# Kernel optimization log

Measured on AMD Instinct MI355X. Metric: run time of the kernel, lower is better.

## Reference

```python
import jax, jax.numpy as jnp
import numpy as np

BN_EPS = 1e-5


def setup_inputs() -> dict:
    key = jax.random.key(0)
    ks = jax.random.split(key, 5)
    B, C, T, V = 64, 64, 300, 25
    O, N = 128, 8  # out_channels, num_adj
    x = jax.random.normal(ks[0], (B, C, T, V), dtype=jnp.float32)
    # adjacency: row-normalized so powers A^1..A^8 stay well-conditioned
    A = jax.random.uniform(ks[1], (V, V), dtype=jnp.float32)
    A = A / jnp.sum(A, axis=1, keepdims=True)
    W = jax.random.normal(ks[2], (N, O // N, C), dtype=jnp.float32) * 0.05  # per-branch 1x1 conv weights
    Wr = jax.random.normal(ks[3], (O, C), dtype=jnp.float32) * 0.05          # residual 1x1 conv weight
    br = jnp.zeros((O,), dtype=jnp.float32)                                   # residual conv bias
    gamma = jnp.ones((O,), dtype=jnp.float32)
    beta = jnp.zeros((O,), dtype=jnp.float32)
    return {"x": x, "A": A, "W": W, "Wr": Wr, "br": br, "gamma": gamma, "beta": beta}


def reference(x, A, W, Wr, br, gamma, beta):
    # x: [B, C, T, V]; A: [V, V]; W: [num_adj, O//num_adj, C]
    num_adj = W.shape[0]
    outs = []
    A_pow = A  # A_list[i] = A^(i+1), matching _split_adjacency_matrix
    for i in range(num_adj):
        g = jnp.einsum('bcfj,jk->bcfk', x, A_pow)           # graph conv on joints
        outs.append(jnp.einsum('oc,bcfk->bofk', W[i], g))   # 1x1 conv (no bias)
        A_pow = A_pow @ A
    out = jnp.concatenate(outs, axis=1)                      # [B, O, T, V]
    residual = jnp.einsum('oc,bcfj->bofj', Wr, x) + br[None, :, None, None]
    out = out + residual
    # BatchNorm2d (training-mode batch statistics over B, T, V per channel)
    mean = jnp.mean(out, axis=(0, 2, 3), keepdims=True)
    var = jnp.var(out, axis=(0, 2, 3), keepdims=True)
    out = gamma[None, :, None, None] * (out - mean) / jnp.sqrt(var + BN_EPS) + beta[None, :, None, None]
    return jax.nn.relu(out)
```

## Files before the change

### kernel.cpp

```cpp
#include <hip/hip_runtime.h>
#include <hip/hip_bf16.h>

#define B_  64
#define C_  64
#define T_  300
#define V_  25
#define O_  128
#define TV  (T_*V_)
#define BTV (B_*T_*V_)
#define NPF 4800
#define HS_STRIDE 258
#define HS_ROWS 107

typedef __bf16 bf16x8 __attribute__((ext_vector_type(8)));
typedef float f32x4 __attribute__((ext_vector_type(4)));

#define WSB_AF    0ull
#define WSB_WT    18432ull
#define WSB_PSC   51200ull
#define WSB_PSQ   2508800ull
#define WSB_P2C   4966400ull
#define WSB_P2Q   5015552ull
#define WSB_SCL   5064704ull
#define WSB_SFT   5065216ull
#define WSB_Y     5065728ull
#define WS_NEED2  127945728ull

static __device__ __forceinline__ unsigned short f2bf(float f) {
    unsigned int u = __float_as_uint(f);
    unsigned int r = (u + 0x7fffu + ((u >> 16) & 1u)) >> 16;
    return (unsigned short)r;
}
static __device__ __forceinline__ float bf2f(unsigned short u) {
    return __uint_as_float(((unsigned int)u) << 16);
}

__global__ __launch_bounds__(256) void k_prep(const float* __restrict__ A,
                                              const float* __restrict__ W,
                                              const float* __restrict__ Wr,
                                              unsigned short* __restrict__ AF,
                                              unsigned short* __restrict__ Wt) {
    const int tid = threadIdx.x;
    if (blockIdx.x == 0) {
        __shared__ float Pall[8][625];
        for (int p = tid; p < 625; p += 256) Pall[0][p] = A[p];
        __syncthreads();
        for (int i = 1; i < 8; i++) {
            for (int p = tid; p < 625; p += 256) {
                int r = p / 25, c = p - r * 25;
                float s = 0.f;
                #pragma unroll 5
                for (int j = 0; j < 25; j++) s = fmaf(Pall[i-1][r*25 + j], A[j*25 + c], s);
                Pall[i][p] = s;
            }
            __syncthreads();
        }
        for (int idx = tid; idx < 18 * 64; idx += 256) {
            int fi = idx >> 6, l = idx & 63, qq = l >> 4, tt = l & 15;
            unsigned short v[8];
            #pragma unroll
            for (int e = 0; e < 8; e++) {
                int j = qq * 8 + e;
                float val = 0.f;
                if (fi < 16) {
                    int i = fi >> 1, k = (fi & 1) * 16 + tt;
                    if (j < 25 && k < 25) val = Pall[i][j * 25 + k];
                } else {
                    int k = (fi - 16) * 16 + tt;
                    if (j < 25 && k < 25 && j == k) val = 1.f;
                }
                v[e] = f2bf(val);
            }
            *(uint4*)(AF + idx * 8) = *(uint4*)v;
        }
    } else {
        const int oc = tid;
        const float* src = (oc < 128) ? (W + oc * 64) : (Wr + (oc - 128) * 64);
        unsigned short row[64];
        #pragma unroll
        for (int c = 0; c < 64; c++) row[c] = f2bf(src[c]);
        #pragma unroll
        for (int cc = 0; cc < 8; cc++)
            *(uint4*)(Wt + oc * 64 + cc * 8) = *(uint4*)(row + cc * 8);
    }
}

__global__ __launch_bounds__(512, 2) void k_fuse(const float* __restrict__ x,
                                                 const unsigned short* __restrict__ Wt,
                                                 const unsigned short* __restrict__ AF,
                                                 unsigned short* __restrict__ Yg,
                                                 float* __restrict__ psc,
                                                 float* __restrict__ psq) {
    __shared__ __align__(16) unsigned short SM[8192 + HS_ROWS * HS_STRIDE];
    unsigned short* As = SM;
    unsigned short* Hs = SM + 8192;
    const int tg = blockIdx.x, b = blockIdx.y;
    const int tid = threadIdx.x, wv = tid >> 6, ln = tid & 63;
    const int q = ln >> 4, t = ln & 15;

    for (int p = tid; p < 1600; p += 512) {
        int c = p / 25, e4 = p - c * 25;
        float4 f = *(const float4*)(x + ((size_t)(b * 64 + c)) * TV + tg * 100 + e4 * 4);
        float vv[4] = { f.x, f.y, f.z, f.w };
        #pragma unroll
        for (int u = 0; u < 4; u++) {
            int r = e4 * 4 + u;
            As[r * 64 + (((c >> 3) ^ (r & 7)) << 3) + (c & 7)] = f2bf(vv[u]);
        }
    }
    for (int w = tid; w < 896; w += 512) ((unsigned int*)As)[3200 + w] = 0u;
    for (int w = tid; w < 903; w += 512) ((unsigned int*)Hs)[12900 + w] = 0u;
    __syncthreads();

    {
        const int rb = wv >> 2, oq = wv & 3;
        f32x4 acc[4][4] = {};
        #pragma unroll
        for (int ks = 0; ks < 2; ks++) {
            const unsigned short* wb = Wt + (oq * 64 + t) * 64 + q * 8 + ks * 32;
            bf16x8 bv[4], af[4];
            #pragma unroll
            for (int ni = 0; ni < 4; ni++) bv[ni] = *(const bf16x8*)(wb + ni * 1024);
            #pragma unroll
            for (int mi = 0; mi < 4; mi++) {
                int row = rb * 64 + mi * 16 + t;
                af[mi] = *(const bf16x8*)(As + row * 64 + (((ks * 4 + q) ^ (row & 7)) << 3));
            }
            #pragma unroll
            for (int mi = 0; mi < 4; mi++)
                #pragma unroll
                for (int ni = 0; ni < 4; ni++)
                    acc[mi][ni] = __builtin_amdgcn_mfma_f32_16x16x32_bf16(bv[ni], af[mi], acc[mi][ni], 0, 0, 0);
        }
        #pragma unroll
        for (int mi = 0; mi < 4; mi++) {
            int row = rb * 64 + mi * 16 + t;
            if (row < 100) {
                #pragma unroll
                for (int ni = 0; ni < 4; ni++) {
                    int co = oq * 64 + ni * 16 + q * 4;
                    unsigned int* dst = (unsigned int*)(Hs + row * HS_STRIDE + co);
                    dst[0] = (unsigned int)f2bf(acc[mi][ni][0]) | ((unsigned int)f2bf(acc[mi][ni][1]) << 16);
                    dst[1] = (unsigned int)f2bf(acc[mi][ni][2]) | ((unsigned int)f2bf(acc[mi][ni][3]) << 16);
                }
            }
        }
    }
    __syncthreads();

    const int s = wv >> 1, bh = wv & 1;
    const bf16x8* AFp = (const bf16x8*)AF;
    const bf16x8 id0 = AFp[16 * 64 + ln];
    const bf16x8 id1 = AFp[17 * 64 + ln];
    f32x4 acc2[4][2];
    #pragma unroll
    for (int ii = 0; ii < 4; ii++) { acc2[ii][0] = (f32x4){0,0,0,0}; acc2[ii][1] = (f32x4){0,0,0,0}; }
    const int rowq = (s * 25 + q * 8) * HS_STRIDE + t;
    #pragma unroll
    for (int ii = 0; ii < 4; ii++) {
        const int i = bh * 4 + ii;
        unsigned short hm[8], hr[8];
        #pragma unroll
        for (int e = 0; e < 8; e++) {
            int a = rowq + e * HS_STRIDE + i * 16;
            hm[e] = Hs[a];
            hr[e] = Hs[a + 128];
        }
        bf16x8 bm = *(bf16x8*)hm;
        bf16x8 brs = *(bf16x8*)hr;
        bf16x8 a0 = AFp[(i * 2 + 0) * 64 + ln];
        bf16x8 a1 = AFp[(i * 2 + 1) * 64 + ln];
        acc2[ii][0] = __builtin_amdgcn_mfma_f32_16x16x32_bf16(id0, brs, acc2[ii][0], 0, 0, 0);
        acc2[ii][1] = __builtin_amdgcn_mfma_f32_16x16x32_bf16(id1, brs, acc2[ii][1], 0, 0, 0);
        acc2[ii][0] = __builtin_amdgcn_mfma_f32_16x16x32_bf16(a0, bm, acc2[ii][0], 0, 0, 0);
        acc2[ii][1] = __builtin_amdgcn_mfma_f32_16x16x32_bf16(a1, bm, acc2[ii][1], 0, 0, 0);
    }
    float* ps = (float*)SM;
    float* qs = ps + 512;
    #pragma unroll
    for (int ii = 0; ii < 4; ii++) {
        float si = 0.f, qi = 0.f;
        #pragma unroll
        for (int mt = 0; mt < 2; mt++)
            #pragma unroll
            for (int r = 0; r < 4; r++) {
                float v = acc2[ii][mt][r];
                si += v; qi += v * v;
            }
        si += __shfl_xor(si, 16); si += __shfl_xor(si, 32);
        qi += __shfl_xor(qi, 16); qi += __shfl_xor(qi, 32);
        if (ln < 16) {
            ps[s * 128 + (bh * 4 + ii) * 16 + t] = si;
            qs[s * 128 + (bh * 4 + ii) * 16 + t] = qi;
        }
    }
    #pragma unroll
    for (int ii = 0; ii < 4; ii++)
        #pragma unroll
        for (int mt = 0; mt < 2; mt++)
            #pragma unroll
            for (int r = 0; r < 4; r++) {
                int k = mt * 16 + q * 4 + r;
                if (k < 25)
                    Hs[(s * 25 + k) * HS_STRIDE + (bh * 4 + ii) * 16 + t] = f2bf(acc2[ii][mt][r]);
            }
    __syncthreads();
    if (tid < 128) {
        float S = ps[tid] + ps[128 + tid] + ps[256 + tid] + ps[384 + tid];
        float Q = qs[tid] + qs[128 + tid] + qs[256 + tid] + qs[384 + tid];
        int blk = b * 75 + tg;
        psc[(size_t)blk * 128 + tid] = S;
        psq[(size_t)blk * 128 + tid] = Q;
    }
    for (int idx = tid; idx < 3200; idx += 512) {
        int o = idx / 25, w = idx - o * 25;
        unsigned short vv[4];
        #pragma unroll
        for (int e = 0; e < 4; e++)
            vv[e] = Hs[(w * 4 + e) * HS_STRIDE + o];
        uint2 d;
        d.x = (unsigned int)vv[0] | ((unsigned int)vv[1] << 16);
        d.y = (unsigned int)vv[2] | ((unsigned int)vv[3] << 16);
        *(uint2*)(Yg + (size_t)(b * 128 + o) * TV + tg * 100 + w * 4) = d;
    }
}

__global__ __launch_bounds__(256) void k_red1(const float* __restrict__ psc,
                                              const float* __restrict__ psq,
                                              float* __restrict__ p2c,
                                              float* __restrict__ p2q) {
    const int r = blockIdx.x;
    const int tid = threadIdx.x;
    const int o = tid & 127;
    const float* src = (tid < 128) ? psc : psq;
    float* dst = (tid < 128) ? p2c : p2q;
    float S = 0.f;
    for (int ii = 0; ii < 50; ii++)
        S += src[(size_t)(r * 50 + ii) * 128 + o];
    dst[r * 128 + o] = S;
}

__global__ void k_fin(const float* __restrict__ p2c, const float* __restrict__ p2q,
                      const float* __restrict__ gamma, const float* __restrict__ beta,
                      float* __restrict__ scale, float* __restrict__ shift) {
    const int o = threadIdx.x;
    if (o >= 128) return;
    float S = 0.f, Q = 0.f;
    for (int r = 0; r < 96; r++) { S += p2c[r * 128 + o]; Q += p2q[r * 128 + o]; }
    float inv = 1.f / (float)BTV;
    float mean = S * inv;
    float var = Q * inv - mean * mean;
    float sc = gamma[o] / sqrtf(var + 1e-5f);
    scale[o] = sc;
    shift[o] = beta[o] - mean * sc;
}

__global__ __launch_bounds__(256) void k_norm2(const unsigned short* __restrict__ Y,
                                               const float* __restrict__ scale,
                                               const float* __restrict__ shift,
                                               float* __restrict__ out) {
    size_t e0 = ((size_t)blockIdx.x * 256 + threadIdx.x) * 8;
    #pragma unroll
    for (int g = 0; g < 2; g++) {
        size_t e = e0 + (size_t)g * 4;
        int o = (int)((e / 7500) & 127);
        float sc = scale[o], sh = shift[o];
        uint2 v = *(const uint2*)(Y + e);
        float4 d;
        d.x = fmaxf(fmaf(bf2f((unsigned short)(v.x & 0xffffu)), sc, sh), 0.f);
        d.y = fmaxf(fmaf(bf2f((unsigned short)(v.x >> 16)),     sc, sh), 0.f);
        d.z = fmaxf(fmaf(bf2f((unsigned short)(v.y & 0xffffu)), sc, sh), 0.f);
        d.w = fmaxf(fmaf(bf2f((unsigned short)(v.y >> 16)),     sc, sh), 0.f);
        *(float4*)(out + e) = d;
    }
}

extern "C" void kernel_launch(void* const* d_in, const int* in_sizes, int n_in,
                              void* d_out, int out_size, void* d_ws, size_t ws_size,
                              hipStream_t stream) {
    const float* x     = (const float*)d_in[0];
    const float* A     = (const float*)d_in[1];
    const float* W     = (const float*)d_in[2];
    const float* Wr    = (const float*)d_in[3];
    const float* gamma = (const float*)d_in[5];
    const float* beta  = (const float*)d_in[6];
    float* out = (float*)d_out;
    char* wsb  = (char*)d_ws;
    if (ws_size < (size_t)WS_NEED2) return;

    unsigned short* AF  = (unsigned short*)(wsb + WSB_AF);
    unsigned short* Wt  = (unsigned short*)(wsb + WSB_WT);
    float*          psc = (float*)(wsb + WSB_PSC);
    float*          psq = (float*)(wsb + WSB_PSQ);
    float*          p2c = (float*)(wsb + WSB_P2C);
    float*          p2q = (float*)(wsb + WSB_P2Q);
    float*          scl = (float*)(wsb + WSB_SCL);
    float*          sft = (float*)(wsb + WSB_SFT);
    unsigned short* Y   = (unsigned short*)(wsb + WSB_Y);

    k_prep<<<2, 256, 0, stream>>>(A, W, Wr, AF, Wt);
    k_fuse<<<dim3(75, 64), 512, 0, stream>>>(x, Wt, AF, Y, psc, psq);
    k_red1<<<96, 256, 0, stream>>>(psc, psq, p2c, p2q);
    k_fin<<<1, 128, 0, stream>>>(p2c, p2q, gamma, beta, scl, sft);
    k_norm2<<<30000, 256, 0, stream>>>(Y, scl, sft, out);
}
```

Measured before the change: 220.3 us.

## Fuse conv, BN statistics and normalization into one cooperative persistent kernel

Replaces the four-kernel pipeline (fused conv, two-stage stats reduction, finalize, normalize) with one cooperative kernel of 480 persistent blocks, each handling 10 tiles. Each block keeps its bf16 conv outputs in registers, writes partial BN sums, crosses a grid-wide barrier, reduces the statistics itself, then normalizes and writes the output. This removes the bf16 intermediate Y round-trip through global memory and three kernel launches. In exchange it adds heavy register pressure from holding 10 tiles of results, needs 480 blocks co-resident under launch bounds of 4 blocks per CU, and pays for a grid sync. If the cooperative launch fails, it falls back to the old kernels.

```diff
diff --git a/kernel.cpp b/kernel.cpp
--- a/kernel.cpp
+++ b/kernel.cpp
@@ -1,5 +1,8 @@
 #include <hip/hip_runtime.h>
 #include <hip/hip_bf16.h>
+#include <hip/hip_cooperative_groups.h>
+
+namespace cg = cooperative_groups;
 
 #define B_  64
 #define C_  64
@@ -8,9 +11,10 @@
 #define O_  128
 #define TV  (T_*V_)
 #define BTV (B_*T_*V_)
-#define NPF 4800
 #define HS_STRIDE 258
 #define HS_ROWS 107
+#define NBLK 480
+#define TILES_PB 10
 
 typedef __bf16 bf16x8 __attribute__((ext_vector_type(8)));
 typedef float f32x4 __attribute__((ext_vector_type(4)));
@@ -82,6 +86,201 @@
         #pragma unroll
         for (int cc = 0; cc < 8; cc++)
             *(uint4*)(Wt + oc * 64 + cc * 8) = *(uint4*)(row + cc * 8);
+    }
+}
+
+__global__ __launch_bounds__(512, 4) void k_mega(const float* __restrict__ x,
+                                                 const unsigned short* __restrict__ Wt,
+                                                 const unsigned short* __restrict__ AF,
+                                                 const float* __restrict__ gamma,
+                                                 const float* __restrict__ beta,
+                                                 float* __restrict__ psc,
+                                                 float* __restrict__ psq,
+                                                 float* __restrict__ out) {
+    __shared__ __align__(16) unsigned short SM[8192 + HS_ROWS * HS_STRIDE];
+    __shared__ float scl[128], sft[128];
+    unsigned short* As = SM;
+    unsigned short* Hs = SM + 8192;
+    const int tid = threadIdx.x, wv = tid >> 6, ln = tid & 63;
+    const int q = ln >> 4, t = ln & 15;
+    const int s = wv >> 1, bh = wv & 1;
+    const bf16x8* AFp = (const bf16x8*)AF;
+    const bf16x8 id0 = AFp[16 * 64 + ln];
+    const bf16x8 id1 = AFp[17 * 64 + ln];
+    const int tile0 = blockIdx.x * TILES_PB;
+
+    for (int w = tid; w < 896; w += 512) ((unsigned int*)As)[3200 + w] = 0u;
+    for (int w = tid; w < 903; w += 512) ((unsigned int*)Hs)[12900 + w] = 0u;
+
+    float sacc[4] = {0.f, 0.f, 0.f, 0.f}, qacc[4] = {0.f, 0.f, 0.f, 0.f};
+    uint2 y[TILES_PB][4][2];
+
+    #pragma unroll
+    for (int tl = 0; tl < TILES_PB; tl++) {
+        const int tile = tile0 + tl;
+        const int b = tile / 75, tg = tile - b * 75;
+        __syncthreads();
+        for (int p = tid; p < 1600; p += 512) {
+            int c = p / 25, e4 = p - c * 25;
+            float4 f = *(const float4*)(x + ((size_t)(b * 64 + c)) * TV + tg * 100 + e4 * 4);
+            float vv[4] = { f.x, f.y, f.z, f.w };
+            #pragma unroll
+            for (int u = 0; u < 4; u++) {
+                int r = e4 * 4 + u;
+                As[r * 64 + (((c >> 3) ^ (r & 7)) << 3) + (c & 7)] = f2bf(vv[u]);
+            }
+        }
+        __syncthreads();
+        {
+            const int rb = wv >> 2, oq = wv & 3;
+            f32x4 acc[4][4] = {};
+            #pragma unroll
+            for (int ks = 0; ks < 2; ks++) {
+                const unsigned short* wb = Wt + (oq * 64 + t) * 64 + q * 8 + ks * 32;
+                bf16x8 bv[4], af[4];
+                #pragma unroll
+                for (int ni = 0; ni < 4; ni++) bv[ni] = *(const bf16x8*)(wb + ni * 1024);
+                #pragma unroll
+                for (int mi = 0; mi < 4; mi++) {
+                    int row = rb * 64 + mi * 16 + t;
+                    af[mi] = *(const bf16x8*)(As + row * 64 + (((ks * 4 + q) ^ (row & 7)) << 3));
+                }
+                #pragma unroll
+                for (int mi = 0; mi < 4; mi++)
+                    #pragma unroll
+                    for (int ni = 0; ni < 4; ni++)
+                        acc[mi][ni] = __builtin_amdgcn_mfma_f32_16x16x32_bf16(bv[ni], af[mi], acc[mi][ni], 0, 0, 0);
+            }
+            #pragma unroll
+            for (int mi = 0; mi < 4; mi++) {
+                int row = rb * 64 + mi * 16 + t;
+                if (row < 100) {
+                    #pragma unroll
+                    for (int ni = 0; ni < 4; ni++) {
+                        int co = oq * 64 + ni * 16 + q * 4;
+                        unsigned int* dst = (unsigned int*)(Hs + row * HS_STRIDE + co);
+                        dst[0] = (unsigned int)f2bf(acc[mi][ni][0]) | ((unsigned int)f2bf(acc[mi][ni][1]) << 16);
+                        dst[1] = (unsigned int)f2bf(acc[mi][ni][2]) | ((unsigned int)f2bf(acc[mi][ni][3]) << 16);
+                    }
+                }
+            }
+        }
+        __syncthreads();
+        {
+            f32x4 acc2[4][2];
+            #pragma unroll
+            for (int ii = 0; ii < 4; ii++) { acc2[ii][0] = (f32x4){0,0,0,0}; acc2[ii][1] = (f32x4){0,0,0,0}; }
+            const int rowq = (s * 25 + q * 8) * HS_STRIDE + t;
+            #pragma unroll
+            for (int ii = 0; ii < 4; ii++) {
+                const int i = bh * 4 + ii;
+                unsigned short hm[8], hr[8];
+                #pragma unroll
+                for (int e = 0; e < 8; e++) {
+                    int a = rowq + e * HS_STRIDE + i * 16;
+                    hm[e] = Hs[a];
+                    hr[e] = Hs[a + 128];
+                }
+                bf16x8 bm = *(bf16x8*)hm;
+                bf16x8 brs = *(bf16x8*)hr;
+                bf16x8 a0 = AFp[(i * 2 + 0) * 64 + ln];
+                bf16x8 a1 = AFp[(i * 2 + 1) * 64 + ln];
+                acc2[ii][0] = __builtin_amdgcn_mfma_f32_16x16x32_bf16(id0, brs, acc2[ii][0], 0, 0, 0);
+                acc2[ii][1] = __builtin_amdgcn_mfma_f32_16x16x32_bf16(id1, brs, acc2[ii][1], 0, 0, 0);
+                acc2[ii][0] = __builtin_amdgcn_mfma_f32_16x16x32_bf16(a0, bm, acc2[ii][0], 0, 0, 0);
+                acc2[ii][1] = __builtin_amdgcn_mfma_f32_16x16x32_bf16(a1, bm, acc2[ii][1], 0, 0, 0);
+            }
+            #pragma unroll
+            for (int ii = 0; ii < 4; ii++) {
+                float si = 0.f, qi = 0.f;
+                #pragma unroll
+                for (int mt = 0; mt < 2; mt++) {
+                    #pragma unroll
+                    for (int r = 0; r < 4; r++) {
+                        float v = acc2[ii][mt][r];
+                        si += v; qi += v * v;
+                    }
+                    y[tl][ii][mt].x = (unsigned int)f2bf(acc2[ii][mt][0]) | ((unsigned int)f2bf(acc2[ii][mt][1]) << 16);
+                    y[tl][ii][mt].y = (unsigned int)f2bf(acc2[ii][mt][2]) | ((unsigned int)f2bf(acc2[ii][mt][3]) << 16);
+                }
+                sacc[ii] += si; qacc[ii] += qi;
+            }
+        }
+    }
+
+    __syncthreads();
+    float* ps = (float*)SM;
+    float* qs = ps + 512;
+    #pragma unroll
+    for (int ii = 0; ii < 4; ii++) {
+        float si = sacc[ii], qi = qacc[ii];
+        si += __shfl_xor(si, 16); si += __shfl_xor(si, 32);
+        qi += __shfl_xor(qi, 16); qi += __shfl_xor(qi, 32);
+        if (ln < 16) {
+            ps[s * 128 + (bh * 4 + ii) * 16 + t] = si;
+            qs[s * 128 + (bh * 4 + ii) * 16 + t] = qi;
+        }
+    }
+    __syncthreads();
+    if (tid < 128) {
+        psc[blockIdx.x * 128 + tid] = ps[tid] + ps[128 + tid] + ps[256 + tid] + ps[384 + tid];
+        psq[blockIdx.x * 128 + tid] = qs[tid] + qs[128 + tid] + qs[256 + tid] + qs[384 + tid];
+    }
+
+    cg::this_grid().sync();
+
+    {
+        const int o = tid & 127, ph = tid >> 7;
+        float S = 0.f, Q = 0.f;
+        for (int i = ph; i < NBLK; i += 4) {
+            S += psc[i * 128 + o];
+            Q += psq[i * 128 + o];
+        }
+        ps[ph * 128 + o] = S;
+        qs[ph * 128 + o] = Q;
+        __syncthreads();
+        if (tid < 128) {
+            float St = ps[tid] + ps[128 + tid] + ps[256 + tid] + ps[384 + tid];
+            float Qt = qs[tid] + qs[128 + tid] + qs[256 + tid] + qs[384 + tid];
+            float inv = 1.f / (float)BTV;
+            float mean = St * inv;
+            float var = Qt * inv - mean * mean;
+            float sc = gamma[tid] / sqrtf(var + 1e-5f);
+            scl[tid] = sc;
+            sft[tid] = beta[tid] - mean * sc;
+        }
+    }
+
+    #pragma unroll
+    for (int tl = 0; tl < TILES_PB; tl++) {
+        const int tile = tile0 + tl;
+        const int b = tile / 75, tg = tile - b * 75;
+        __syncthreads();
+        #pragma unroll
+        for (int ii = 0; ii < 4; ii++)
+            #pragma unroll
+            for (int mt = 0; mt < 2; mt++) {
+                unsigned int lo = y[tl][ii][mt].x, hi = y[tl][ii][mt].y;
+                unsigned short vr[4] = { (unsigned short)(lo & 0xffffu), (unsigned short)(lo >> 16),
+                                         (unsigned short)(hi & 0xffffu), (unsigned short)(hi >> 16) };
+                #pragma unroll
+                for (int r = 0; r < 4; r++) {
+                    int k = mt * 16 + q * 4 + r;
+                    if (k < 25)
+                        Hs[(s * 25 + k) * HS_STRIDE + (bh * 4 + ii) * 16 + t] = vr[r];
+                }
+            }
+        __syncthreads();
+        for (int idx = tid; idx < 3200; idx += 512) {
+            int o = idx / 25, w = idx - o * 25;
+            float sc = scl[o], sh = sft[o];
+            float4 d;
+            float* dp = (float*)&d;
+            #pragma unroll
+            for (int e = 0; e < 4; e++)
+                dp[e] = fmaxf(fmaf(bf2f(Hs[(w * 4 + e) * HS_STRIDE + o]), sc, sh), 0.f);
+            *(float4*)(out + (size_t)(b * 128 + o) * TV + tg * 100 + w * 4) = d;
+        }
     }
 }
 
@@ -111,7 +310,6 @@
     for (int w = tid; w < 896; w += 512) ((unsigned int*)As)[3200 + w] = 0u;
     for (int w = tid; w < 903; w += 512) ((unsigned int*)Hs)[12900 + w] = 0u;
     __syncthreads();
-
     {
         const int rb = wv >> 2, oq = wv & 3;
         f32x4 acc[4][4] = {};
@@ -147,7 +345,6 @@
         }
     }
     __syncthreads();
-
     const int s = wv >> 1, bh = wv & 1;
     const bf16x8* AFp = (const bf16x8*)AF;
     const bf16x8 id0 = AFp[16 * 64 + ln];
@@ -299,8 +496,15 @@
     unsigned short* Y   = (unsigned short*)(wsb + WSB_Y);
 
     k_prep<<<2, 256, 0, stream>>>(A, W, Wr, AF, Wt);
-    k_fuse<<<dim3(75, 64), 512, 0, stream>>>(x, Wt, AF, Y, psc, psq);
-    k_red1<<<96, 256, 0, stream>>>(psc, psq, p2c, p2q);
-    k_fin<<<1, 128, 0, stream>>>(p2c, p2q, gamma, beta, scl, sft);
-    k_norm2<<<30000, 256, 0, stream>>>(Y, scl, sft, out);
-}
+
+    void* args[] = { (void*)&x, (void*)&Wt, (void*)&AF, (void*)&gamma, (void*)&beta,
+                     (void*)&psc, (void*)&psq, (void*)&out };
+    hipError_t err = hipLaunchCooperativeKernel((const void*)k_mega, dim3(NBLK), dim3(512),
+                                                args, 0, stream);
+    if (err != hipSuccess) {
+        k_fuse<<<dim3(75, 64), 512, 0, stream>>>(x, Wt, AF, Y, psc, psq);
+        k_red1<<<96, 256, 0, stream>>>(psc, psq, p2c, p2q);
+        k_fin<<<1, 128, 0, stream>>>(p2c, p2q, gamma, beta, scl, sft);
+        k_norm2<<<30000, 256, 0, stream>>>(Y, scl, sft, out);
+    }
+}
```

Measured after the change: 503.7 us. 2.29x slower.

## Halve fused tile to 2 frames per block and merge stat reductions into one kernel

Applied to the files above, without the earlier changes.

The fused conv kernel now processes 50 time-joint rows per 256-thread block instead of 100 rows per 512-thread block. The grid doubles to 150x64 blocks with half the shared memory, which should allow more resident blocks and finer scheduling. The two-stage partial-sum reduction (k_red1 plus a single-block k_fin) is replaced by one 128-block kernel that reduces all 9600 partials per channel with wave shuffles, cutting a launch. In exchange, the partial-stat buffer doubles in size, the global stores are narrower (32-bit instead of 64-bit), and the MFMA tiles are partly padded because only 50 of 64 rows are valid.

```diff
diff --git a/kernel.cpp b/kernel.cpp
--- a/kernel.cpp
+++ b/kernel.cpp
@@ -8,9 +8,9 @@
 #define O_  128
 #define TV  (T_*V_)
 #define BTV (B_*T_*V_)
-#define NPF 4800
 #define HS_STRIDE 258
-#define HS_ROWS 107
+#define HS_ROWS 57
+#define NPF 9600
 
 typedef __bf16 bf16x8 __attribute__((ext_vector_type(8)));
 typedef float f32x4 __attribute__((ext_vector_type(4)));
@@ -18,13 +18,11 @@
 #define WSB_AF    0ull
 #define WSB_WT    18432ull
 #define WSB_PSC   51200ull
-#define WSB_PSQ   2508800ull
-#define WSB_P2C   4966400ull
-#define WSB_P2Q   5015552ull
-#define WSB_SCL   5064704ull
-#define WSB_SFT   5065216ull
-#define WSB_Y     5065728ull
-#define WS_NEED2  127945728ull
+#define WSB_PSQ   4966400ull
+#define WSB_SCL   9881600ull
+#define WSB_SFT   9882112ull
+#define WSB_Y     9882624ull
+#define WS_NEED2  132762624ull
 
 static __device__ __forceinline__ unsigned short f2bf(float f) {
     unsigned int u = __float_as_uint(f);
@@ -85,35 +83,32 @@
     }
 }
 
-__global__ __launch_bounds__(512, 2) void k_fuse(const float* __restrict__ x,
+__global__ __launch_bounds__(256, 4) void k_fuse(const float* __restrict__ x,
                                                  const unsigned short* __restrict__ Wt,
                                                  const unsigned short* __restrict__ AF,
                                                  unsigned short* __restrict__ Yg,
                                                  float* __restrict__ psc,
                                                  float* __restrict__ psq) {
-    __shared__ __align__(16) unsigned short SM[8192 + HS_ROWS * HS_STRIDE];
+    __shared__ __align__(16) unsigned short SM[4096 + HS_ROWS * HS_STRIDE];
     unsigned short* As = SM;
-    unsigned short* Hs = SM + 8192;
+    unsigned short* Hs = SM + 4096;
     const int tg = blockIdx.x, b = blockIdx.y;
     const int tid = threadIdx.x, wv = tid >> 6, ln = tid & 63;
     const int q = ln >> 4, t = ln & 15;
 
-    for (int p = tid; p < 1600; p += 512) {
-        int c = p / 25, e4 = p - c * 25;
-        float4 f = *(const float4*)(x + ((size_t)(b * 64 + c)) * TV + tg * 100 + e4 * 4);
-        float vv[4] = { f.x, f.y, f.z, f.w };
-        #pragma unroll
-        for (int u = 0; u < 4; u++) {
-            int r = e4 * 4 + u;
-            As[r * 64 + (((c >> 3) ^ (r & 7)) << 3) + (c & 7)] = f2bf(vv[u]);
-        }
-    }
-    for (int w = tid; w < 896; w += 512) ((unsigned int*)As)[3200 + w] = 0u;
-    for (int w = tid; w < 903; w += 512) ((unsigned int*)Hs)[12900 + w] = 0u;
+    for (int p = tid; p < 1600; p += 256) {
+        int c = p / 25, e = p - c * 25;
+        float2 f = *(const float2*)(x + ((size_t)(b * 64 + c)) * TV + tg * 50 + e * 2);
+        int r0 = e * 2;
+        As[r0 * 64 + (((c >> 3) ^ (r0 & 7)) << 3) + (c & 7)]         = f2bf(f.x);
+        As[(r0+1) * 64 + (((c >> 3) ^ ((r0+1) & 7)) << 3) + (c & 7)] = f2bf(f.y);
+    }
+    for (int w = tid; w < 448; w += 256) ((unsigned int*)As)[1600 + w] = 0u;
+    for (int w = tid; w < 903; w += 256) ((unsigned int*)Hs)[6450 + w] = 0u;
     __syncthreads();
 
     {
-        const int rb = wv >> 2, oq = wv & 3;
+        const int oq = wv;
         f32x4 acc[4][4] = {};
         #pragma unroll
         for (int ks = 0; ks < 2; ks++) {
@@ -123,7 +118,7 @@
             for (int ni = 0; ni < 4; ni++) bv[ni] = *(const bf16x8*)(wb + ni * 1024);
             #pragma unroll
             for (int mi = 0; mi < 4; mi++) {
-                int row = rb * 64 + mi * 16 + t;
+                int row = mi * 16 + t;
                 af[mi] = *(const bf16x8*)(As + row * 64 + (((ks * 4 + q) ^ (row & 7)) << 3));
             }
             #pragma unroll
@@ -134,8 +129,8 @@
         }
         #pragma unroll
         for (int mi = 0; mi < 4; mi++) {
-            int row = rb * 64 + mi * 16 + t;
-            if (row < 100) {
+            int row = mi * 16 + t;
+            if (row < 50) {
                 #pragma unroll
                 for (int ni = 0; ni < 4; ni++) {
                     int co = oq * 64 + ni * 16 + q * 4;
@@ -176,7 +171,7 @@
         acc2[ii][1] = __builtin_amdgcn_mfma_f32_16x16x32_bf16(a1, bm, acc2[ii][1], 0, 0, 0);
     }
     float* ps = (float*)SM;
-    float* qs = ps + 512;
+    float* qs = ps + 256;
     #pragma unroll
     for (int ii = 0; ii < 4; ii++) {
         float si = 0.f, qi = 0.f;
@@ -206,53 +201,48 @@
             }
     __syncthreads();
     if (tid < 128) {
-        float S = ps[tid] + ps[128 + tid] + ps[256 + tid] + ps[384 + tid];
-        float Q = qs[tid] + qs[128 + tid] + qs[256 + tid] + qs[384 + tid];
-        int blk = b * 75 + tg;
+        float S = ps[tid] + ps[128 + tid];
+        float Q = qs[tid] + qs[128 + tid];
+        int blk = b * 150 + tg;
         psc[(size_t)blk * 128 + tid] = S;
         psq[(size_t)blk * 128 + tid] = Q;
     }
-    for (int idx = tid; idx < 3200; idx += 512) {
+    for (int idx = tid; idx < 3200; idx += 256) {
         int o = idx / 25, w = idx - o * 25;
-        unsigned short vv[4];
-        #pragma unroll
-        for (int e = 0; e < 4; e++)
-            vv[e] = Hs[(w * 4 + e) * HS_STRIDE + o];
-        uint2 d;
-        d.x = (unsigned int)vv[0] | ((unsigned int)vv[1] << 16);
-        d.y = (unsigned int)vv[2] | ((unsigned int)vv[3] << 16);
-        *(uint2*)(Yg + (size_t)(b * 128 + o) * TV + tg * 100 + w * 4) = d;
-    }
-}
-
-__global__ __launch_bounds__(256) void k_red1(const float* __restrict__ psc,
+        unsigned int d = (unsigned int)Hs[(w * 2) * HS_STRIDE + o]
+                       | ((unsigned int)Hs[(w * 2 + 1) * HS_STRIDE + o] << 16);
+        *(unsigned int*)(Yg + (size_t)(b * 128 + o) * TV + tg * 50 + w * 2) = d;
+    }
+}
+
+__global__ __launch_bounds__(256) void k_fin2(const float* __restrict__ psc,
                                               const float* __restrict__ psq,
-                                              float* __restrict__ p2c,
-                                              float* __restrict__ p2q) {
-    const int r = blockIdx.x;
-    const int tid = threadIdx.x;
-    const int o = tid & 127;
-    const float* src = (tid < 128) ? psc : psq;
-    float* dst = (tid < 128) ? p2c : p2q;
-    float S = 0.f;
-    for (int ii = 0; ii < 50; ii++)
-        S += src[(size_t)(r * 50 + ii) * 128 + o];
-    dst[r * 128 + o] = S;
-}
-
-__global__ void k_fin(const float* __restrict__ p2c, const float* __restrict__ p2q,
-                      const float* __restrict__ gamma, const float* __restrict__ beta,
-                      float* __restrict__ scale, float* __restrict__ shift) {
-    const int o = threadIdx.x;
-    if (o >= 128) return;
+                                              const float* __restrict__ gamma,
+                                              const float* __restrict__ beta,
+                                              float* __restrict__ scale,
+                                              float* __restrict__ shift) {
+    const int o = blockIdx.x, tid = threadIdx.x;
     float S = 0.f, Q = 0.f;
-    for (int r = 0; r < 96; r++) { S += p2c[r * 128 + o]; Q += p2q[r * 128 + o]; }
-    float inv = 1.f / (float)BTV;
-    float mean = S * inv;
-    float var = Q * inv - mean * mean;
-    float sc = gamma[o] / sqrtf(var + 1e-5f);
-    scale[o] = sc;
-    shift[o] = beta[o] - mean * sc;
+    for (int i = tid; i < NPF; i += 256) {
+        S += psc[(size_t)i * 128 + o];
+        Q += psq[(size_t)i * 128 + o];
+    }
+    #pragma unroll
+    for (int m = 1; m < 64; m <<= 1) { S += __shfl_xor(S, m); Q += __shfl_xor(Q, m); }
+    __shared__ float ls[4], lq[4];
+    int w = tid >> 6;
+    if ((tid & 63) == 0) { ls[w] = S; lq[w] = Q; }
+    __syncthreads();
+    if (tid == 0) {
+        float St = ls[0] + ls[1] + ls[2] + ls[3];
+        float Qt = lq[0] + lq[1] + lq[2] + lq[3];
+        float inv = 1.f / (float)BTV;
+        float mean = St * inv;
+        float var = Qt * inv - mean * mean;
+        float sc = gamma[o] / sqrtf(var + 1e-5f);
+        scale[o] = sc;
+        shift[o] = beta[o] - mean * sc;
+    }
 }
 
 __global__ __launch_bounds__(256) void k_norm2(const unsigned short* __restrict__ Y,
@@ -292,15 +282,12 @@
     unsigned short* Wt  = (unsigned short*)(wsb + WSB_WT);
     float*          psc = (float*)(wsb + WSB_PSC);
     float*          psq = (float*)(wsb + WSB_PSQ);
-    float*          p2c = (float*)(wsb + WSB_P2C);
-    float*          p2q = (float*)(wsb + WSB_P2Q);
     float*          scl = (float*)(wsb + WSB_SCL);
     float*          sft = (float*)(wsb + WSB_SFT);
     unsigned short* Y   = (unsigned short*)(wsb + WSB_Y);
 
     k_prep<<<2, 256, 0, stream>>>(A, W, Wr, AF, Wt);
-    k_fuse<<<dim3(75, 64), 512, 0, stream>>>(x, Wt, AF, Y, psc, psq);
-    k_red1<<<96, 256, 0, stream>>>(psc, psq, p2c, p2q);
-    k_fin<<<1, 128, 0, stream>>>(p2c, p2q, gamma, beta, scl, sft);
+    k_fuse<<<dim3(150, 64), 256, 0, stream>>>(x, Wt, AF, Y, psc, psq);
+    k_fin2<<<128, 256, 0, stream>>>(psc, psq, gamma, beta, scl, sft);
     k_norm2<<<30000, 256, 0, stream>>>(Y, scl, sft, out);
 }
```

After: 267.7 us. 21.5% more time.
